# Kernel tuning notes

Hardware: AMD Instinct MI355X
Metric: run time of the kernel (lower is better)

The kernel has to match this reference:

```python
import jax, jax.numpy as jnp
import numpy as np

N_NODES = 100000
KERNEL_SIZE = 2  # per dim, dim=1 -> 2 kernel weight matrices


def spline_conv(x, edge_index, W, root, bias):
    """PyG SplineConv, dim=1, kernel_size=2, degree=1 open B-spline, aggr='mean'.

    edge_attr is ones (built inside the torch forward), clamped to [0,1].
    Open linear B-spline with K=2: v = u*(K-1); idx = clip(floor(v), 0, K-2) == 0;
    frac = v - idx. Basis weights (1-frac, frac) on kernel indices (0, 1).
    """
    src, dst = edge_index[0], edge_index[1]  # messages flow src -> dst
    E = src.shape[0]
    u = jnp.ones((E,), x.dtype)              # edge pseudo-coordinates (clamped ones)
    v = u * (KERNEL_SIZE - 1)
    idx = jnp.clip(jnp.floor(v), 0, KERNEL_SIZE - 2)  # always 0 for K=2
    frac = v - idx                            # in [0,1]
    # Transform all nodes by both kernel weight matrices once: (2, N, out)
    xw = jnp.einsum('ni,kio->kno', x, W)
    # Per-edge basis-weighted message (idx==0 => kernel indices 0 and 1)
    msg = (1.0 - frac)[:, None] * xw[0, src] + frac[:, None] * xw[1, src]
    agg = jax.ops.segment_sum(msg, dst, num_segments=N_NODES)
    deg = jax.ops.segment_sum(jnp.ones((E,), x.dtype), dst, num_segments=N_NODES)
    agg = agg / jnp.clip(deg, 1.0)[:, None]   # mean aggregation
    return agg + x @ root + bias


def setup_inputs() -> dict:
    key = jax.random.key(0)
    ks = jax.random.split(key, 8)
    N, F, H, C, E = N_NODES, 128, 16, 40, 3200000
    x = jax.random.normal(ks[0], (N, F), dtype=jnp.float32)
    edge_index = jax.random.randint(ks[1], (2, E), 0, N, dtype=jnp.int32)
    W1 = jax.random.normal(ks[2], (2, F, H), dtype=jnp.float32) * 0.1
    root1 = jax.random.normal(ks[3], (F, H), dtype=jnp.float32) * 0.1
    b1 = jnp.zeros((H,), dtype=jnp.float32)
    W2 = jax.random.normal(ks[4], (2, H, C), dtype=jnp.float32) * 0.1
    root2 = jax.random.normal(ks[5], (H, C), dtype=jnp.float32) * 0.1
    b2 = jnp.zeros((C,), dtype=jnp.float32)
    return {"x": x, "edge_index": edge_index, "W1": W1, "root1": root1,
            "b1": b1, "W2": W2, "root2": root2, "b2": b2}


def reference(x, edge_index, W1, root1, b1, W2, root2, b2):
    # eval mode: F.dropout(training=False) is identity
    h = jax.nn.elu(spline_conv(x, edge_index, W1, root1, b1))
    out = spline_conv(h, edge_index, W2, root2, b2)
    return jax.nn.log_softmax(out, axis=1)
```

## Files before the change

### kernel.cpp

```cpp
#include <hip/hip_runtime.h>
#include <hip/hip_bf16.h>

#define N_NODES 100000
#define FIN 128
#define HID 16
#define NCLS 40
#define NEDGE 3200000
#define NBUCK 391
#define NCHUNK 782
#define SCAP 12288

typedef int v4i __attribute__((ext_vector_type(4)));
typedef __attribute__((ext_vector_type(8))) short bf16x8;
typedef __attribute__((ext_vector_type(4))) float f32x4;

__device__ __forceinline__ unsigned short f2b(float f) {
  union { float f; unsigned u; } v;
  v.f = f;
  unsigned r = v.u + 0x7FFFu + ((v.u >> 16) & 1u);
  return (unsigned short)(r >> 16);
}

__device__ __forceinline__ void accum8(uint4 w, float* a) {
  union { unsigned u; float f; } t;
  t.u = w.x << 16;         a[0] += t.f;
  t.u = w.x & 0xFFFF0000u; a[1] += t.f;
  t.u = w.y << 16;         a[2] += t.f;
  t.u = w.y & 0xFFFF0000u; a[3] += t.f;
  t.u = w.z << 16;         a[4] += t.f;
  t.u = w.z & 0xFFFF0000u; a[5] += t.f;
  t.u = w.w << 16;         a[6] += t.f;
  t.u = w.w & 0xFFFF0000u; a[7] += t.f;
}

__global__ __launch_bounds__(256) void proj1_kernel(
    const float* __restrict__ x, const float* __restrict__ W1,
    const float* __restrict__ root1,
    unsigned* __restrict__ xw1b, float* __restrict__ xr1) {
  __shared__ unsigned short Wb[2][4][4][16][8];

  int tid = threadIdx.x;
  for (int t = tid; t < 4096; t += 256) {
    int cg = t >> 11;
    int rem = t & 2047;
    int kb = rem >> 9;
    int g = (rem >> 7) & 3;
    int c = (rem >> 3) & 15;
    int i = rem & 7;
    int k = kb * 32 + g * 8 + i;
    float v = (cg == 0) ? W1[FIN * HID + k * HID + c] : root1[k * HID + c];
    Wb[cg][kb][g][c][i] = f2b(v);
  }
  __syncthreads();

  int wid = tid >> 6;
  int lane = tid & 63;
  int n0 = blockIdx.x * 64 + wid * 16;
  if (n0 >= N_NODES) return;

  int row = lane & 15;
  int g = lane >> 4;
  const float* xp = x + (size_t)(n0 + row) * FIN + g * 8;

  bf16x8 afr[4];
#pragma unroll
  for (int kb = 0; kb < 4; ++kb) {
    float4 u0 = *(const float4*)(xp + kb * 32);
    float4 u1 = *(const float4*)(xp + kb * 32 + 4);
    bf16x8 a;
    a[0] = (short)f2b(u0.x);
    a[1] = (short)f2b(u0.y);
    a[2] = (short)f2b(u0.z);
    a[3] = (short)f2b(u0.w);
    a[4] = (short)f2b(u1.x);
    a[5] = (short)f2b(u1.y);
    a[6] = (short)f2b(u1.z);
    a[7] = (short)f2b(u1.w);
    afr[kb] = a;
  }

  f32x4 c0 = {0.f, 0.f, 0.f, 0.f};
  f32x4 c1 = {0.f, 0.f, 0.f, 0.f};
#pragma unroll
  for (int kb = 0; kb < 4; ++kb) {
    bf16x8 b0 = *(const bf16x8*)&Wb[0][kb][g][row][0];
    c0 = __builtin_amdgcn_mfma_f32_16x16x32_bf16(afr[kb], b0, c0, 0, 0, 0);
  }
#pragma unroll
  for (int kb = 0; kb < 4; ++kb) {
    bf16x8 b1 = *(const bf16x8*)&Wb[1][kb][g][row][0];
    c1 = __builtin_amdgcn_mfma_f32_16x16x32_bf16(afr[kb], b1, c1, 0, 0, 0);
  }

  int col = lane & 15;
  unsigned short* xwu = (unsigned short*)xw1b;
#pragma unroll
  for (int r = 0; r < 4; ++r) {
    int n = n0 + g * 4 + r;
    xwu[(size_t)n * HID + col] = f2b(c1[r] * 0.f + c0[r]);
    xr1[(size_t)n * HID + col] = c1[r];
  }
}

__global__ __launch_bounds__(512) void histB_kernel(
    const int* __restrict__ dst, int* __restrict__ bcnt) {
  __shared__ int hc[NBUCK];
  for (int t = threadIdx.x; t < NBUCK; t += 512) hc[t] = 0;
  __syncthreads();
  int e0 = blockIdx.x * 4096 + threadIdx.x * 8;
  if (e0 + 8 <= NEDGE) {
    int4 a = *(const int4*)(dst + e0);
    int4 b = *(const int4*)(dst + e0 + 4);
    atomicAdd(&hc[a.x >> 8], 1);
    atomicAdd(&hc[a.y >> 8], 1);
    atomicAdd(&hc[a.z >> 8], 1);
    atomicAdd(&hc[a.w >> 8], 1);
    atomicAdd(&hc[b.x >> 8], 1);
    atomicAdd(&hc[b.y >> 8], 1);
    atomicAdd(&hc[b.z >> 8], 1);
    atomicAdd(&hc[b.w >> 8], 1);
  } else {
    for (int e = e0; e < NEDGE; ++e) atomicAdd(&hc[dst[e] >> 8], 1);
  }
  __syncthreads();
  for (int t = threadIdx.x; t < NBUCK; t += 512) {
    int v = hc[t];
    if (v) atomicAdd(&bcnt[t], v);
  }
}

__global__ __launch_bounds__(512) void scan_kernel(
    const int* __restrict__ bcnt, int* __restrict__ boff,
    int* __restrict__ gcursor, int* __restrict__ rowptr) {
  __shared__ int s[512];
  int v = (threadIdx.x < NBUCK) ? bcnt[threadIdx.x] : 0;
  s[threadIdx.x] = v;
  __syncthreads();
  for (int off = 1; off < 512; off <<= 1) {
    int t = (threadIdx.x >= off) ? s[threadIdx.x - off] : 0;
    __syncthreads();
    s[threadIdx.x] += t;
    __syncthreads();
  }
  if (threadIdx.x < NBUCK) {
    int e = s[threadIdx.x] - v;
    boff[threadIdx.x] = e;
    gcursor[threadIdx.x] = e;
  }
  if (threadIdx.x == 0) {
    boff[NBUCK] = NEDGE;
    rowptr[N_NODES] = NEDGE;
  }
}

__global__ __launch_bounds__(512) void partA_kernel(
    const int* __restrict__ src, const int* __restrict__ dst,
    int* __restrict__ gcursor, unsigned* __restrict__ recs) {
  __shared__ int cnt[NBUCK];
  __shared__ int start[NBUCK];
  __shared__ int base[NBUCK];
  __shared__ int scn[512];
  __shared__ unsigned srec[4096];
  __shared__ unsigned short sbk[4096];

  int tid = threadIdx.x;
  for (int t = tid; t < NBUCK; t += 512) cnt[t] = 0;
  __syncthreads();

  int ebase = blockIdx.x * 4096;
  int nblk = NEDGE - ebase;
  if (nblk > 4096) nblk = 4096;

  unsigned recv[8];
  int bk[8];
  int rank[8];
  int e0 = ebase + tid * 8;
  if (e0 + 8 <= NEDGE) {
    int4 d0 = *(const int4*)(dst + e0);
    int4 d1 = *(const int4*)(dst + e0 + 4);
    int4 s0 = *(const int4*)(src + e0);
    int4 s1 = *(const int4*)(src + e0 + 4);
    int dv[8] = {d0.x, d0.y, d0.z, d0.w, d1.x, d1.y, d1.z, d1.w};
    int sv[8] = {s0.x, s0.y, s0.z, s0.w, s1.x, s1.y, s1.z, s1.w};
#pragma unroll
    for (int k = 0; k < 8; ++k) {
      bk[k] = dv[k] >> 8;
      recv[k] = (unsigned)sv[k] | ((unsigned)(dv[k] & 255) << 17);
      rank[k] = atomicAdd(&cnt[bk[k]], 1);
    }
  } else {
#pragma unroll
    for (int k = 0; k < 8; ++k) {
      int e = e0 + k;
      if (e < NEDGE) {
        int d = dst[e];
        bk[k] = d >> 8;
        recv[k] = (unsigned)src[e] | ((unsigned)(d & 255) << 17);
        rank[k] = atomicAdd(&cnt[bk[k]], 1);
      } else {
        bk[k] = -1;
      }
    }
  }
  __syncthreads();

  int v = (tid < NBUCK) ? cnt[tid] : 0;
  scn[tid] = v;
  __syncthreads();
  for (int off = 1; off < 512; off <<= 1) {
    int t = (tid >= off) ? scn[tid - off] : 0;
    __syncthreads();
    scn[tid] += t;
    __syncthreads();
  }
  if (tid < NBUCK) {
    start[tid] = scn[tid] - v;
    base[tid] = v ? atomicAdd(&gcursor[tid], v) : 0;
  }
  __syncthreads();

#pragma unroll
  for (int k = 0; k < 8; ++k) {
    if (bk[k] >= 0) {
      int pos = start[bk[k]] + rank[k];
      srec[pos] = recv[k];
      sbk[pos] = (unsigned short)bk[k];
    }
  }
  __syncthreads();

  for (int i = tid; i < nblk; i += 512) {
    int b = sbk[i];
    recs[base[b] + (i - start[b])] = srec[i];
  }
}

__global__ __launch_bounds__(1024) void sortB_kernel(
    const int* __restrict__ boff, const unsigned* __restrict__ recs,
    int* __restrict__ rowptr, int* __restrict__ colsrc) {
  __shared__ int hist[256];
  __shared__ int s[256];
  __shared__ int cur[256];
  __shared__ int staged[SCAP];
  if (threadIdx.x < 256) hist[threadIdx.x] = 0;
  __syncthreads();

  int b = blockIdx.x;
  int beg = boff[b], end = boff[b + 1];
  for (int j = beg + threadIdx.x; j < end; j += 1024)
    atomicAdd(&hist[recs[j] >> 17], 1);
  __syncthreads();

  if (threadIdx.x < 256) s[threadIdx.x] = hist[threadIdx.x];
  __syncthreads();
  for (int off = 1; off < 256; off <<= 1) {
    int t = 0;
    if (threadIdx.x < 256 && threadIdx.x >= off) t = s[threadIdx.x - off];
    __syncthreads();
    if (threadIdx.x < 256) s[threadIdx.x] += t;
    __syncthreads();
  }
  if (threadIdx.x < 256) {
    int excl = s[threadIdx.x] - hist[threadIdx.x];
    int n = b * 256 + threadIdx.x;
    if (n < N_NODES) rowptr[n] = beg + excl;
    cur[threadIdx.x] = excl;
  }
  __syncthreads();

  for (int j = beg + threadIdx.x; j < end; j += 1024) {
    unsigned r = recs[j];
    int dl = r >> 17;
    int pos = atomicAdd(&cur[dl], 1);
    if (pos < SCAP) staged[pos] = (int)(r & 0x1FFFF);
    else colsrc[beg + pos] = (int)(r & 0x1FFFF);
  }
  __syncthreads();

  int size = end - beg;
  if (size > SCAP) size = SCAP;
  for (int i = threadIdx.x; i < size; i += 1024) colsrc[beg + i] = staged[i];
}

__global__ __launch_bounds__(256) void gather1_kernel(
    const int* __restrict__ rowptr, const int* __restrict__ colsrc,
    const uint4* __restrict__ valb8, const float4* __restrict__ xr14,
    const float* __restrict__ b1, float4* __restrict__ h4,
    uint4* __restrict__ hb8) {
  int t = blockIdx.x * 256 + threadIdx.x;
  int n = t >> 3;
  if (n >= N_NODES) return;
  int d = t & 1;
  int p = (t >> 1) & 3;
  int beg = rowptr[n], end = rowptr[n + 1];

  float a[8] = {0.f, 0.f, 0.f, 0.f, 0.f, 0.f, 0.f, 0.f};
  int bA = (beg + 3) & ~3;
  int eA = end & ~3;
  if (bA > eA) {
    if (p == 0)
      for (int j = beg; j < end; ++j) accum8(valb8[colsrc[j] * 2 + d], a);
  } else {
    if (p == 0) {
      for (int j = beg; j < bA; ++j) accum8(valb8[colsrc[j] * 2 + d], a);
    } else if (p == 3) {
      for (int j = eA; j < end; ++j) accum8(valb8[colsrc[j] * 2 + d], a);
    }
    float a1[8] = {0.f, 0.f, 0.f, 0.f, 0.f, 0.f, 0.f, 0.f};
    int j = bA + p * 4;
    for (; j + 20 <= eA; j += 32) {
      v4i c0 = __builtin_nontemporal_load((const v4i*)(colsrc + j));
      v4i c1 = __builtin_nontemporal_load((const v4i*)(colsrc + j + 16));
      uint4 w0 = valb8[c0.x * 2 + d];
      uint4 w1 = valb8[c0.y * 2 + d];
      uint4 w2 = valb8[c0.z * 2 + d];
      uint4 w3 = valb8[c0.w * 2 + d];
      uint4 w4 = valb8[c1.x * 2 + d];
      uint4 w5 = valb8[c1.y * 2 + d];
      uint4 w6 = valb8[c1.z * 2 + d];
      uint4 w7 = valb8[c1.w * 2 + d];
      accum8(w0, a);
      accum8(w1, a1);
      accum8(w2, a);
      accum8(w3, a1);
      accum8(w4, a);
      accum8(w5, a1);
      accum8(w6, a);
      accum8(w7, a1);
    }
    for (; j + 4 <= eA; j += 16) {
      v4i c0 = __builtin_nontemporal_load((const v4i*)(colsrc + j));
      accum8(valb8[c0.x * 2 + d], a);
      accum8(valb8[c0.y * 2 + d], a1);
      accum8(valb8[c0.z * 2 + d], a);
      accum8(valb8[c0.w * 2 + d], a1);
    }
#pragma unroll
    for (int k = 0; k < 8; ++k) a[k] += a1[k];
  }

#pragma unroll
  for (int k = 0; k < 8; ++k) {
    a[k] += __shfl_xor(a[k], 2);
    a[k] += __shfl_xor(a[k], 4);
  }
  if (p) return;

  float inv = 1.0f / fmaxf((float)(end - beg), 1.0f);
  float4 r0 = xr14[n * 4 + 2 * d];
  float4 r1 = xr14[n * 4 + 2 * d + 1];
  const float4* bb = (const float4*)b1;
  float4 bb0 = bb[2 * d], bb1 = bb[2 * d + 1];
  float o[8];
  o[0] = a[0] * inv + r0.x + bb0.x;
  o[1] = a[1] * inv + r0.y + bb0.y;
  o[2] = a[2] * inv + r0.z + bb0.z;
  o[3] = a[3] * inv + r0.w + bb0.w;
  o[4] = a[4] * inv + r1.x + bb1.x;
  o[5] = a[5] * inv + r1.y + bb1.y;
  o[6] = a[6] * inv + r1.z + bb1.z;
  o[7] = a[7] * inv + r1.w + bb1.w;
#pragma unroll
  for (int k = 0; k < 8; ++k) o[k] = (o[k] > 0.f) ? o[k] : expm1f(o[k]);
  h4[n * 4 + 2 * d] = make_float4(o[0], o[1], o[2], o[3]);
  h4[n * 4 + 2 * d + 1] = make_float4(o[4], o[5], o[6], o[7]);
  uint4 pk;
  pk.x = (unsigned)f2b(o[0]) | ((unsigned)f2b(o[1]) << 16);
  pk.y = (unsigned)f2b(o[2]) | ((unsigned)f2b(o[3]) << 16);
  pk.z = (unsigned)f2b(o[4]) | ((unsigned)f2b(o[5]) << 16);
  pk.w = (unsigned)f2b(o[6]) | ((unsigned)f2b(o[7]) << 16);
  hb8[n * 2 + d] = pk;
}

__global__ __launch_bounds__(256) void gather2_kernel(
    const int* __restrict__ rowptr, const int* __restrict__ colsrc,
    const uint4* __restrict__ valb8, float4* __restrict__ agg2n4) {
  int t = blockIdx.x * 256 + threadIdx.x;
  int n = t >> 3;
  if (n >= N_NODES) return;
  int d = t & 1;
  int p = (t >> 1) & 3;
  int beg = rowptr[n], end = rowptr[n + 1];

  float a[8] = {0.f, 0.f, 0.f, 0.f, 0.f, 0.f, 0.f, 0.f};
  int bA = (beg + 3) & ~3;
  int eA = end & ~3;
  if (bA > eA) {
    if (p == 0)
      for (int j = beg; j < end; ++j) accum8(valb8[colsrc[j] * 2 + d], a);
  } else {
    if (p == 0) {
      for (int j = beg; j < bA; ++j) accum8(valb8[colsrc[j] * 2 + d], a);
    } else if (p == 3) {
      for (int j = eA; j < end; ++j) accum8(valb8[colsrc[j] * 2 + d], a);
    }
    float a1[8] = {0.f, 0.f, 0.f, 0.f, 0.f, 0.f, 0.f, 0.f};
    int j = bA + p * 4;
    for (; j + 20 <= eA; j += 32) {
      v4i c0 = __builtin_nontemporal_load((const v4i*)(colsrc + j));
      v4i c1 = __builtin_nontemporal_load((const v4i*)(colsrc + j + 16));
      uint4 w0 = valb8[c0.x * 2 + d];
      uint4 w1 = valb8[c0.y * 2 + d];
      uint4 w2 = valb8[c0.z * 2 + d];
      uint4 w3 = valb8[c0.w * 2 + d];
      uint4 w4 = valb8[c1.x * 2 + d];
      uint4 w5 = valb8[c1.y * 2 + d];
      uint4 w6 = valb8[c1.z * 2 + d];
      uint4 w7 = valb8[c1.w * 2 + d];
      accum8(w0, a);
      accum8(w1, a1);
      accum8(w2, a);
      accum8(w3, a1);
      accum8(w4, a);
      accum8(w5, a1);
      accum8(w6, a);
      accum8(w7, a1);
    }
    for (; j + 4 <= eA; j += 16) {
      v4i c0 = __builtin_nontemporal_load((const v4i*)(colsrc + j));
      accum8(valb8[c0.x * 2 + d], a);
      accum8(valb8[c0.y * 2 + d], a1);
      accum8(valb8[c0.z * 2 + d], a);
      accum8(valb8[c0.w * 2 + d], a1);
    }
#pragma unroll
    for (int k = 0; k < 8; ++k) a[k] += a1[k];
  }

#pragma unroll
  for (int k = 0; k < 8; ++k) {
    a[k] += __shfl_xor(a[k], 2);
    a[k] += __shfl_xor(a[k], 4);
  }
  if (p) return;

  float inv = 1.0f / fmaxf((float)(end - beg), 1.0f);
  agg2n4[n * 4 + 2 * d] =
      make_float4(a[0] * inv, a[1] * inv, a[2] * inv, a[3] * inv);
  agg2n4[n * 4 + 2 * d + 1] =
      make_float4(a[4] * inv, a[5] * inv, a[6] * inv, a[7] * inv);
}

__global__ __launch_bounds__(256) void out_kernel(
    const float* __restrict__ h, const float* __restrict__ agg2n,
    const float* __restrict__ W2, const float* __restrict__ root2,
    const float* __restrict__ b2v, float* __restrict__ out) {
  __shared__ float Wl[HID * NCLS];
  __shared__ float Rl[HID * NCLS];
  __shared__ float Bl[NCLS];
  for (int i = threadIdx.x; i < HID * NCLS; i += blockDim.x) {
    Wl[i] = W2[HID * NCLS + i];
    Rl[i] = root2[i];
  }
  if (threadIdx.x < NCLS) Bl[threadIdx.x] = b2v[threadIdx.x];
  __syncthreads();

  int n = blockIdx.x * blockDim.x + threadIdx.x;
  if (n >= N_NODES) return;

  float hv[HID], av[HID];
#pragma unroll
  for (int c = 0; c < HID; ++c) {
    hv[c] = h[n * HID + c];
    av[c] = agg2n[n * HID + c];
  }
  float logit[NCLS];
#pragma unroll
  for (int j = 0; j < NCLS; ++j) logit[j] = Bl[j];
  for (int c = 0; c < HID; ++c) {
    float hc = hv[c], ac = av[c];
#pragma unroll
    for (int j = 0; j < NCLS; ++j)
      logit[j] += ac * Wl[c * NCLS + j] + hc * Rl[c * NCLS + j];
  }
  float m = -INFINITY;
#pragma unroll
  for (int j = 0; j < NCLS; ++j) m = fmaxf(m, logit[j]);
  float s = 0.f;
#pragma unroll
  for (int j = 0; j < NCLS; ++j) s += expf(logit[j] - m);
  float lse = m + logf(s);
#pragma unroll
  for (int j = 0; j < NCLS; ++j)
    out[(size_t)n * NCLS + j] = logit[j] - lse;
}

extern "C" void kernel_launch(void* const* d_in, const int* in_sizes, int n_in,
                              void* d_out, int out_size, void* d_ws,
                              size_t ws_size, hipStream_t stream) {
  const float* x = (const float*)d_in[0];
  const int* ei = (const int*)d_in[1];
  const float* W1 = (const float*)d_in[2];
  const float* root1 = (const float*)d_in[3];
  const float* b1 = (const float*)d_in[4];
  const float* W2 = (const float*)d_in[5];
  const float* root2 = (const float*)d_in[6];
  const float* b2v = (const float*)d_in[7];
  float* out = (float*)d_out;

  const int* src = ei;
  const int* dstp = ei + NEDGE;

  char* w = (char*)d_ws;
  int* bcnt = (int*)w;           w += 2048;
  int* boff = (int*)w;           w += 2048;
  int* gcursor = (int*)w;        w += 2048;
  int* rowptr = (int*)w;         w += (size_t)(N_NODES + 4) * 4;
  unsigned* recs = (unsigned*)w; w += (size_t)NEDGE * 4;
  int* colsrc = (int*)w;         w += (size_t)NEDGE * 4;
  unsigned* xw1b = (unsigned*)w; w += (size_t)N_NODES * HID * 2;
  float* xr1 = (float*)w;        w += (size_t)N_NODES * HID * 4;
  unsigned short* hb = (unsigned short*)w; w += (size_t)N_NODES * HID * 2;

  float* h = (float*)recs;
  float* agg2n = (float*)((char*)recs + (size_t)N_NODES * HID * 4);

  hipMemsetAsync(bcnt, 0, 2048, stream);

  proj1_kernel<<<(N_NODES + 63) / 64, 256, 0, stream>>>(x, W1, root1, xw1b,
                                                        xr1);
  histB_kernel<<<NCHUNK, 512, 0, stream>>>(dstp, bcnt);
  scan_kernel<<<1, 512, 0, stream>>>(bcnt, boff, gcursor, rowptr);
  partA_kernel<<<NCHUNK, 512, 0, stream>>>(src, dstp, gcursor, recs);
  sortB_kernel<<<NBUCK, 1024, 0, stream>>>(boff, recs, rowptr, colsrc);
  gather1_kernel<<<(N_NODES * 8 + 255) / 256, 256, 0, stream>>>(
      rowptr, colsrc, (const uint4*)xw1b, (const float4*)xr1, b1, (float4*)h,
      (uint4*)hb);
  gather2_kernel<<<(N_NODES * 8 + 255) / 256, 256, 0, stream>>>(
      rowptr, colsrc, (const uint4*)hb, (float4*)agg2n);
  out_kernel<<<(N_NODES + 255) / 256, 256, 0, stream>>>(h, agg2n, W2, root2,
                                                        b2v, out);
}
```

Before: 257.2 us.

## Fuse projection into partition kernel and fuse second gather with output softmax

The bf16 MFMA projection moves into the edge-partition launch as extra blocks, so both run concurrently in one grid and one launch disappears. The second-layer gather is merged with the output linear layer and log-softmax, spreading each node's 40 logits over 8 threads that reduce with shuffles. This removes the fp32 h and agg2 round-trips through global memory. As a trade-off, the root term of layer 2 now reads the bf16 copy of h instead of fp32, which lowers precision slightly.

```diff
diff --git a/kernel.cpp b/kernel.cpp
--- a/kernel.cpp
+++ b/kernel.cpp
@@ -8,6 +8,7 @@
 #define NEDGE 3200000
 #define NBUCK 391
 #define NCHUNK 782
+#define PROJB 782
 #define SCAP 12288
 
 typedef int v4i __attribute__((ext_vector_type(4)));
@@ -31,75 +32,6 @@
   t.u = w.z & 0xFFFF0000u; a[5] += t.f;
   t.u = w.w << 16;         a[6] += t.f;
   t.u = w.w & 0xFFFF0000u; a[7] += t.f;
-}
-
-__global__ __launch_bounds__(256) void proj1_kernel(
-    const float* __restrict__ x, const float* __restrict__ W1,
-    const float* __restrict__ root1,
-    unsigned* __restrict__ xw1b, float* __restrict__ xr1) {
-  __shared__ unsigned short Wb[2][4][4][16][8];
-
-  int tid = threadIdx.x;
-  for (int t = tid; t < 4096; t += 256) {
-    int cg = t >> 11;
-    int rem = t & 2047;
-    int kb = rem >> 9;
-    int g = (rem >> 7) & 3;
-    int c = (rem >> 3) & 15;
-    int i = rem & 7;
-    int k = kb * 32 + g * 8 + i;
-    float v = (cg == 0) ? W1[FIN * HID + k * HID + c] : root1[k * HID + c];
-    Wb[cg][kb][g][c][i] = f2b(v);
-  }
-  __syncthreads();
-
-  int wid = tid >> 6;
-  int lane = tid & 63;
-  int n0 = blockIdx.x * 64 + wid * 16;
-  if (n0 >= N_NODES) return;
-
-  int row = lane & 15;
-  int g = lane >> 4;
-  const float* xp = x + (size_t)(n0 + row) * FIN + g * 8;
-
-  bf16x8 afr[4];
-#pragma unroll
-  for (int kb = 0; kb < 4; ++kb) {
-    float4 u0 = *(const float4*)(xp + kb * 32);
-    float4 u1 = *(const float4*)(xp + kb * 32 + 4);
-    bf16x8 a;
-    a[0] = (short)f2b(u0.x);
-    a[1] = (short)f2b(u0.y);
-    a[2] = (short)f2b(u0.z);
-    a[3] = (short)f2b(u0.w);
-    a[4] = (short)f2b(u1.x);
-    a[5] = (short)f2b(u1.y);
-    a[6] = (short)f2b(u1.z);
-    a[7] = (short)f2b(u1.w);
-    afr[kb] = a;
-  }
-
-  f32x4 c0 = {0.f, 0.f, 0.f, 0.f};
-  f32x4 c1 = {0.f, 0.f, 0.f, 0.f};
-#pragma unroll
-  for (int kb = 0; kb < 4; ++kb) {
-    bf16x8 b0 = *(const bf16x8*)&Wb[0][kb][g][row][0];
-    c0 = __builtin_amdgcn_mfma_f32_16x16x32_bf16(afr[kb], b0, c0, 0, 0, 0);
-  }
-#pragma unroll
-  for (int kb = 0; kb < 4; ++kb) {
-    bf16x8 b1 = *(const bf16x8*)&Wb[1][kb][g][row][0];
-    c1 = __builtin_amdgcn_mfma_f32_16x16x32_bf16(afr[kb], b1, c1, 0, 0, 0);
-  }
-
-  int col = lane & 15;
-  unsigned short* xwu = (unsigned short*)xw1b;
-#pragma unroll
-  for (int r = 0; r < 4; ++r) {
-    int n = n0 + g * 4 + r;
-    xwu[(size_t)n * HID + col] = f2b(c1[r] * 0.f + c0[r]);
-    xr1[(size_t)n * HID + col] = c1[r];
-  }
 }
 
 __global__ __launch_bounds__(512) void histB_kernel(
@@ -153,85 +85,154 @@
   }
 }
 
-__global__ __launch_bounds__(512) void partA_kernel(
+__global__ __launch_bounds__(512) void mid_kernel(
     const int* __restrict__ src, const int* __restrict__ dst,
-    int* __restrict__ gcursor, unsigned* __restrict__ recs) {
-  __shared__ int cnt[NBUCK];
-  __shared__ int start[NBUCK];
-  __shared__ int base[NBUCK];
-  __shared__ int scn[512];
-  __shared__ unsigned srec[4096];
-  __shared__ unsigned short sbk[4096];
-
+    int* __restrict__ gcursor, unsigned* __restrict__ recs,
+    const float* __restrict__ x, const float* __restrict__ W1,
+    const float* __restrict__ root1,
+    unsigned* __restrict__ xw1b, float* __restrict__ xr1) {
+  __shared__ __attribute__((aligned(16))) char smem[31328];
   int tid = threadIdx.x;
-  for (int t = tid; t < NBUCK; t += 512) cnt[t] = 0;
-  __syncthreads();
-
-  int ebase = blockIdx.x * 4096;
-  int nblk = NEDGE - ebase;
-  if (nblk > 4096) nblk = 4096;
-
-  unsigned recv[8];
-  int bk[8];
-  int rank[8];
-  int e0 = ebase + tid * 8;
-  if (e0 + 8 <= NEDGE) {
-    int4 d0 = *(const int4*)(dst + e0);
-    int4 d1 = *(const int4*)(dst + e0 + 4);
-    int4 s0 = *(const int4*)(src + e0);
-    int4 s1 = *(const int4*)(src + e0 + 4);
-    int dv[8] = {d0.x, d0.y, d0.z, d0.w, d1.x, d1.y, d1.z, d1.w};
-    int sv[8] = {s0.x, s0.y, s0.z, s0.w, s1.x, s1.y, s1.z, s1.w};
+
+  if (blockIdx.x < NCHUNK) {
+    int* cnt = (int*)smem;
+    int* start = (int*)(smem + 1568);
+    int* base = (int*)(smem + 3136);
+    int* scn = (int*)(smem + 4704);
+    unsigned* srec = (unsigned*)(smem + 6752);
+    unsigned short* sbk = (unsigned short*)(smem + 23136);
+
+    for (int t = tid; t < NBUCK; t += 512) cnt[t] = 0;
+    __syncthreads();
+
+    int ebase = blockIdx.x * 4096;
+    int nblk = NEDGE - ebase;
+    if (nblk > 4096) nblk = 4096;
+
+    unsigned recv[8];
+    int bk[8];
+    int rank[8];
+    int e0 = ebase + tid * 8;
+    if (e0 + 8 <= NEDGE) {
+      int4 d0 = *(const int4*)(dst + e0);
+      int4 d1 = *(const int4*)(dst + e0 + 4);
+      int4 s0 = *(const int4*)(src + e0);
+      int4 s1 = *(const int4*)(src + e0 + 4);
+      int dv[8] = {d0.x, d0.y, d0.z, d0.w, d1.x, d1.y, d1.z, d1.w};
+      int sv[8] = {s0.x, s0.y, s0.z, s0.w, s1.x, s1.y, s1.z, s1.w};
+#pragma unroll
+      for (int k = 0; k < 8; ++k) {
+        bk[k] = dv[k] >> 8;
+        recv[k] = (unsigned)sv[k] | ((unsigned)(dv[k] & 255) << 17);
+        rank[k] = atomicAdd(&cnt[bk[k]], 1);
+      }
+    } else {
+#pragma unroll
+      for (int k = 0; k < 8; ++k) {
+        int e = e0 + k;
+        if (e < NEDGE) {
+          int d = dst[e];
+          bk[k] = d >> 8;
+          recv[k] = (unsigned)src[e] | ((unsigned)(d & 255) << 17);
+          rank[k] = atomicAdd(&cnt[bk[k]], 1);
+        } else {
+          bk[k] = -1;
+        }
+      }
+    }
+    __syncthreads();
+
+    int v = (tid < NBUCK) ? cnt[tid] : 0;
+    scn[tid] = v;
+    __syncthreads();
+    for (int off = 1; off < 512; off <<= 1) {
+      int t = (tid >= off) ? scn[tid - off] : 0;
+      __syncthreads();
+      scn[tid] += t;
+      __syncthreads();
+    }
+    if (tid < NBUCK) {
+      start[tid] = scn[tid] - v;
+      base[tid] = v ? atomicAdd(&gcursor[tid], v) : 0;
+    }
+    __syncthreads();
+
 #pragma unroll
     for (int k = 0; k < 8; ++k) {
-      bk[k] = dv[k] >> 8;
-      recv[k] = (unsigned)sv[k] | ((unsigned)(dv[k] & 255) << 17);
-      rank[k] = atomicAdd(&cnt[bk[k]], 1);
+      if (bk[k] >= 0) {
+        int pos = start[bk[k]] + rank[k];
+        srec[pos] = recv[k];
+        sbk[pos] = (unsigned short)bk[k];
+      }
+    }
+    __syncthreads();
+
+    for (int i = tid; i < nblk; i += 512) {
+      int b = sbk[i];
+      recs[base[b] + (i - start[b])] = srec[i];
     }
   } else {
-#pragma unroll
-    for (int k = 0; k < 8; ++k) {
-      int e = e0 + k;
-      if (e < NEDGE) {
-        int d = dst[e];
-        bk[k] = d >> 8;
-        recv[k] = (unsigned)src[e] | ((unsigned)(d & 255) << 17);
-        rank[k] = atomicAdd(&cnt[bk[k]], 1);
-      } else {
-        bk[k] = -1;
-      }
-    }
-  }
-  __syncthreads();
-
-  int v = (tid < NBUCK) ? cnt[tid] : 0;
-  scn[tid] = v;
-  __syncthreads();
-  for (int off = 1; off < 512; off <<= 1) {
-    int t = (tid >= off) ? scn[tid - off] : 0;
-    __syncthreads();
-    scn[tid] += t;
-    __syncthreads();
-  }
-  if (tid < NBUCK) {
-    start[tid] = scn[tid] - v;
-    base[tid] = v ? atomicAdd(&gcursor[tid], v) : 0;
-  }
-  __syncthreads();
-
-#pragma unroll
-  for (int k = 0; k < 8; ++k) {
-    if (bk[k] >= 0) {
-      int pos = start[bk[k]] + rank[k];
-      srec[pos] = recv[k];
-      sbk[pos] = (unsigned short)bk[k];
-    }
-  }
-  __syncthreads();
-
-  for (int i = tid; i < nblk; i += 512) {
-    int b = sbk[i];
-    recs[base[b] + (i - start[b])] = srec[i];
+    unsigned short* Wb = (unsigned short*)smem;
+    for (int t = tid; t < 4096; t += 512) {
+      int cg = t >> 11;
+      int rem = t & 2047;
+      int kb = rem >> 9;
+      int g = (rem >> 7) & 3;
+      int c = (rem >> 3) & 15;
+      int i = rem & 7;
+      int k = kb * 32 + g * 8 + i;
+      float v = (cg == 0) ? W1[FIN * HID + k * HID + c] : root1[k * HID + c];
+      Wb[((((cg * 4 + kb) * 4 + g) * 16) + c) * 8 + i] = f2b(v);
+    }
+    __syncthreads();
+
+    int wid = tid >> 6;
+    int lane = tid & 63;
+    int n0 = (blockIdx.x - NCHUNK) * 128 + wid * 16;
+    if (n0 >= N_NODES) return;
+
+    int row = lane & 15;
+    int g = lane >> 4;
+    const float* xp = x + (size_t)(n0 + row) * FIN + g * 8;
+
+    bf16x8 afr[4];
+#pragma unroll
+    for (int kb = 0; kb < 4; ++kb) {
+      float4 u0 = *(const float4*)(xp + kb * 32);
+      float4 u1 = *(const float4*)(xp + kb * 32 + 4);
+      bf16x8 a;
+      a[0] = (short)f2b(u0.x);
+      a[1] = (short)f2b(u0.y);
+      a[2] = (short)f2b(u0.z);
+      a[3] = (short)f2b(u0.w);
+      a[4] = (short)f2b(u1.x);
+      a[5] = (short)f2b(u1.y);
+      a[6] = (short)f2b(u1.z);
+      a[7] = (short)f2b(u1.w);
+      afr[kb] = a;
+    }
+
+    f32x4 c0 = {0.f, 0.f, 0.f, 0.f};
+    f32x4 c1 = {0.f, 0.f, 0.f, 0.f};
+#pragma unroll
+    for (int kb = 0; kb < 4; ++kb) {
+      bf16x8 b0 = *(const bf16x8*)&Wb[(((0 * 4 + kb) * 4 + g) * 16 + row) * 8];
+      c0 = __builtin_amdgcn_mfma_f32_16x16x32_bf16(afr[kb], b0, c0, 0, 0, 0);
+    }
+#pragma unroll
+    for (int kb = 0; kb < 4; ++kb) {
+      bf16x8 b1 = *(const bf16x8*)&Wb[(((1 * 4 + kb) * 4 + g) * 16 + row) * 8];
+      c1 = __builtin_amdgcn_mfma_f32_16x16x32_bf16(afr[kb], b1, c1, 0, 0, 0);
+    }
+
+    int col = lane & 15;
+    unsigned short* xwu = (unsigned short*)xw1b;
+#pragma unroll
+    for (int r = 0; r < 4; ++r) {
+      int n = n0 + g * 4 + r;
+      xwu[(size_t)n * HID + col] = f2b(c0[r]);
+      xr1[(size_t)n * HID + col] = c1[r];
+    }
   }
 }
 
@@ -285,8 +286,7 @@
 __global__ __launch_bounds__(256) void gather1_kernel(
     const int* __restrict__ rowptr, const int* __restrict__ colsrc,
     const uint4* __restrict__ valb8, const float4* __restrict__ xr14,
-    const float* __restrict__ b1, float4* __restrict__ h4,
-    uint4* __restrict__ hb8) {
+    const float* __restrict__ b1, uint4* __restrict__ hb8) {
   int t = blockIdx.x * 256 + threadIdx.x;
   int n = t >> 3;
   if (n >= N_NODES) return;
@@ -362,8 +362,6 @@
   o[7] = a[7] * inv + r1.w + bb1.w;
 #pragma unroll
   for (int k = 0; k < 8; ++k) o[k] = (o[k] > 0.f) ? o[k] : expm1f(o[k]);
-  h4[n * 4 + 2 * d] = make_float4(o[0], o[1], o[2], o[3]);
-  h4[n * 4 + 2 * d + 1] = make_float4(o[4], o[5], o[6], o[7]);
   uint4 pk;
   pk.x = (unsigned)f2b(o[0]) | ((unsigned)f2b(o[1]) << 16);
   pk.y = (unsigned)f2b(o[2]) | ((unsigned)f2b(o[3]) << 16);
@@ -372,14 +370,37 @@
   hb8[n * 2 + d] = pk;
 }
 
-__global__ __launch_bounds__(256) void gather2_kernel(
+__global__ __launch_bounds__(256) void g2out_kernel(
     const int* __restrict__ rowptr, const int* __restrict__ colsrc,
-    const uint4* __restrict__ valb8, float4* __restrict__ agg2n4) {
-  int t = blockIdx.x * 256 + threadIdx.x;
-  int n = t >> 3;
-  if (n >= N_NODES) return;
-  int d = t & 1;
-  int p = (t >> 1) & 3;
+    const uint4* __restrict__ valb8, const unsigned* __restrict__ hbu,
+    const float* __restrict__ W2, const float* __restrict__ root2,
+    const float* __restrict__ b2v, float* __restrict__ out) {
+  __shared__ float aggl[32][17];
+  __shared__ float hl[32][17];
+  __shared__ float Wl[HID * NCLS];
+  __shared__ float Rl[HID * NCLS];
+  __shared__ float Bl[NCLS];
+
+  int tid = threadIdx.x;
+  for (int i = tid; i < HID * NCLS; i += 256) {
+    Wl[i] = W2[HID * NCLS + i];
+    Rl[i] = root2[i];
+  }
+  if (tid < NCLS) Bl[tid] = b2v[tid];
+  {
+    unsigned u = hbu[(size_t)blockIdx.x * 256 + tid];
+    union { unsigned u; float f; } lo, hi;
+    lo.u = u << 16;
+    hi.u = u & 0xFFFF0000u;
+    int nl = tid >> 3, uu = tid & 7;
+    hl[nl][uu * 2] = lo.f;
+    hl[nl][uu * 2 + 1] = hi.f;
+  }
+
+  int nl = tid >> 3;
+  int n = blockIdx.x * 32 + nl;
+  int d = tid & 1;
+  int p = (tid >> 1) & 3;
   int beg = rowptr[n], end = rowptr[n + 1];
 
   float a[8] = {0.f, 0.f, 0.f, 0.f, 0.f, 0.f, 0.f, 0.f};
@@ -432,57 +453,41 @@
     a[k] += __shfl_xor(a[k], 2);
     a[k] += __shfl_xor(a[k], 4);
   }
-  if (p) return;
-
-  float inv = 1.0f / fmaxf((float)(end - beg), 1.0f);
-  agg2n4[n * 4 + 2 * d] =
-      make_float4(a[0] * inv, a[1] * inv, a[2] * inv, a[3] * inv);
-  agg2n4[n * 4 + 2 * d + 1] =
-      make_float4(a[4] * inv, a[5] * inv, a[6] * inv, a[7] * inv);
-}
-
-__global__ __launch_bounds__(256) void out_kernel(
-    const float* __restrict__ h, const float* __restrict__ agg2n,
-    const float* __restrict__ W2, const float* __restrict__ root2,
-    const float* __restrict__ b2v, float* __restrict__ out) {
-  __shared__ float Wl[HID * NCLS];
-  __shared__ float Rl[HID * NCLS];
-  __shared__ float Bl[NCLS];
-  for (int i = threadIdx.x; i < HID * NCLS; i += blockDim.x) {
-    Wl[i] = W2[HID * NCLS + i];
-    Rl[i] = root2[i];
-  }
-  if (threadIdx.x < NCLS) Bl[threadIdx.x] = b2v[threadIdx.x];
-  __syncthreads();
-
-  int n = blockIdx.x * blockDim.x + threadIdx.x;
-  if (n >= N_NODES) return;
-
-  float hv[HID], av[HID];
-#pragma unroll
+  if (p == 0) {
+    float inv = 1.0f / fmaxf((float)(end - beg), 1.0f);
+#pragma unroll
+    for (int k = 0; k < 8; ++k) aggl[nl][d * 8 + k] = a[k] * inv;
+  }
+  __syncthreads();
+
+  int q = tid & 7;
+  float lg[5];
+#pragma unroll
+  for (int jj = 0; jj < 5; ++jj) lg[jj] = Bl[q * 5 + jj];
   for (int c = 0; c < HID; ++c) {
-    hv[c] = h[n * HID + c];
-    av[c] = agg2n[n * HID + c];
-  }
-  float logit[NCLS];
-#pragma unroll
-  for (int j = 0; j < NCLS; ++j) logit[j] = Bl[j];
-  for (int c = 0; c < HID; ++c) {
-    float hc = hv[c], ac = av[c];
-#pragma unroll
-    for (int j = 0; j < NCLS; ++j)
-      logit[j] += ac * Wl[c * NCLS + j] + hc * Rl[c * NCLS + j];
-  }
-  float m = -INFINITY;
-#pragma unroll
-  for (int j = 0; j < NCLS; ++j) m = fmaxf(m, logit[j]);
+    float ac = aggl[nl][c];
+    float hc = hl[nl][c];
+    const float* wrow = Wl + c * NCLS + q * 5;
+    const float* rrow = Rl + c * NCLS + q * 5;
+#pragma unroll
+    for (int jj = 0; jj < 5; ++jj) lg[jj] += ac * wrow[jj] + hc * rrow[jj];
+  }
+  float m = lg[0];
+#pragma unroll
+  for (int jj = 1; jj < 5; ++jj) m = fmaxf(m, lg[jj]);
+  m = fmaxf(m, __shfl_xor(m, 1));
+  m = fmaxf(m, __shfl_xor(m, 2));
+  m = fmaxf(m, __shfl_xor(m, 4));
   float s = 0.f;
 #pragma unroll
-  for (int j = 0; j < NCLS; ++j) s += expf(logit[j] - m);
+  for (int jj = 0; jj < 5; ++jj) s += expf(lg[jj] - m);
+  s += __shfl_xor(s, 1);
+  s += __shfl_xor(s, 2);
+  s += __shfl_xor(s, 4);
   float lse = m + logf(s);
-#pragma unroll
-  for (int j = 0; j < NCLS; ++j)
-    out[(size_t)n * NCLS + j] = logit[j] - lse;
+  float* op = out + (size_t)n * NCLS + q * 5;
+#pragma unroll
+  for (int jj = 0; jj < 5; ++jj) op[jj] = lg[jj] - lse;
 }
 
 extern "C" void kernel_launch(void* const* d_in, const int* in_sizes, int n_in,
@@ -512,22 +517,16 @@
   float* xr1 = (float*)w;        w += (size_t)N_NODES * HID * 4;
   unsigned short* hb = (unsigned short*)w; w += (size_t)N_NODES * HID * 2;
 
-  float* h = (float*)recs;
-  float* agg2n = (float*)((char*)recs + (size_t)N_NODES * HID * 4);
-
   hipMemsetAsync(bcnt, 0, 2048, stream);
 
-  proj1_kernel<<<(N_NODES + 63) / 64, 256, 0, stream>>>(x, W1, root1, xw1b,
-                                                        xr1);
   histB_kernel<<<NCHUNK, 512, 0, stream>>>(dstp, bcnt);
   scan_kernel<<<1, 512, 0, stream>>>(bcnt, boff, gcursor, rowptr);
-  partA_kernel<<<NCHUNK, 512, 0, stream>>>(src, dstp, gcursor, recs);
+  mid_kernel<<<NCHUNK + PROJB, 512, 0, stream>>>(src, dstp, gcursor, recs, x,
+                                                 W1, root1, xw1b, xr1);
   sortB_kernel<<<NBUCK, 1024, 0, stream>>>(boff, recs, rowptr, colsrc);
   gather1_kernel<<<(N_NODES * 8 + 255) / 256, 256, 0, stream>>>(
-      rowptr, colsrc, (const uint4*)xw1b, (const float4*)xr1, b1, (float4*)h,
-      (uint4*)hb);
-  gather2_kernel<<<(N_NODES * 8 + 255) / 256, 256, 0, stream>>>(
-      rowptr, colsrc, (const uint4*)hb, (float4*)agg2n);
-  out_kernel<<<(N_NODES + 255) / 256, 256, 0, stream>>>(h, agg2n, W2, root2,
-                                                        b2v, out);
-}
+      rowptr, colsrc, (const uint4*)xw1b, (const float4*)xr1, b1, (uint4*)hb);
+  g2out_kernel<<<N_NODES / 32, 256, 0, stream>>>(
+      rowptr, colsrc, (const uint4*)hb, (const unsigned*)hb, W2, root2, b2v,
+      out);
+}
```

Result: faster. 242.9 us (-5.6%).
